# Kernel optimization log

Hardware: AMD Instinct MI355X
Metric: run time of the kernel (lower is better)

The kernel has to match this reference:

```python
import jax, jax.numpy as jnp
import numpy as np

EMBED_DIM = 1024
N_HEADS = 16
N_KV_HEADS = 4
HEAD_DIM = EMBED_DIM // N_HEADS  # 64
N_GROUPS = N_HEADS // N_KV_HEADS  # 4
COPE_MAX_LEN = 64


def setup_inputs() -> dict:
    key = jax.random.key(0)
    ks = jax.random.split(key, 16)
    B, T = 4, 1024
    s = 0.02
    return {
        "query": jax.random.normal(ks[0], (B, T, EMBED_DIM), jnp.float32),
        "key": jax.random.normal(ks[1], (B, T, EMBED_DIM), jnp.float32),
        "value": jax.random.normal(ks[2], (B, T, EMBED_DIM), jnp.float32),
        "wq": jax.random.normal(ks[3], (EMBED_DIM, EMBED_DIM), jnp.float32) * s,
        "bq": jnp.zeros((EMBED_DIM,), jnp.float32),
        "wk": jax.random.normal(ks[4], (HEAD_DIM * N_KV_HEADS, EMBED_DIM), jnp.float32) * s,
        "bk": jnp.zeros((HEAD_DIM * N_KV_HEADS,), jnp.float32),
        "wv": jax.random.normal(ks[5], (HEAD_DIM * N_KV_HEADS, EMBED_DIM), jnp.float32) * s,
        "bv": jnp.zeros((HEAD_DIM * N_KV_HEADS,), jnp.float32),
        "wo": jax.random.normal(ks[6], (EMBED_DIM, EMBED_DIM), jnp.float32) * s,
        "bo": jnp.zeros((EMBED_DIM,), jnp.float32),
        "pos_emb": jax.random.normal(ks[7], (HEAD_DIM, COPE_MAX_LEN), jnp.float32) * s,
    }


def _cope_bias(q, sim, pos_emb):
    # q: [b,g,h,i,d], sim: [b,g,h,i,j], pos_emb: [d, M]
    gates = jax.nn.sigmoid(sim)
    # reversed cumulative sum over keys -> contextual positions
    pos = jnp.flip(jnp.cumsum(jnp.flip(gates, -1), axis=-1), -1)
    pos = jnp.clip(pos, 0.0, COPE_MAX_LEN - 1)
    pos_floor = jnp.floor(pos)
    w = pos - pos_floor  # interpolation weight
    logits_int = jnp.einsum('bghid,dm->bghim', q, pos_emb)  # [b,g,h,i,M]
    lo = jnp.take_along_axis(logits_int, pos_floor.astype(jnp.int32), axis=-1)
    hi = jnp.take_along_axis(logits_int, jnp.ceil(pos).astype(jnp.int32), axis=-1)
    return hi * w + lo * (1.0 - w)


def reference(query, key, value, wq, bq, wk, bk, wv, bv, wo, bo, pos_emb):
    B, Tq, E = query.shape
    Tk = key.shape[1]
    temp = jnp.sqrt(jnp.float32(HEAD_DIM))
    q = (query @ wq.T + bq).reshape(B, Tq, N_HEADS, HEAD_DIM).transpose(0, 2, 1, 3)
    k = (key @ wk.T + bk).reshape(B, Tk, N_KV_HEADS, HEAD_DIM).transpose(0, 2, 1, 3)
    v = (value @ wv.T + bv).reshape(B, Tk, N_KV_HEADS, HEAD_DIM).transpose(0, 2, 1, 3)
    qg = q.reshape(B, N_GROUPS, N_KV_HEADS, Tq, HEAD_DIM)
    sim = jnp.einsum('bghid,bhjd->bghij', qg, k) / temp
    attn_weights = sim + _cope_bias(qg, sim, pos_emb)
    attn_probs = jax.nn.softmax(attn_weights.astype(jnp.float32), axis=-1).astype(attn_weights.dtype)
    out = jnp.einsum('bghij,bhjd->bghid', attn_probs, v)
    # b g h i d -> b i (g h) d -> b i E
    out = out.transpose(0, 3, 1, 2, 4).reshape(B, Tq, E)
    return out @ wo.T + bo
```

## Files before the change

kernel.cpp:

```cpp
#include <hip/hip_runtime.h>
#include <hip/hip_bf16.h>
#include <stdint.h>

typedef unsigned short u16;
typedef __attribute__((ext_vector_type(8))) short short8;
typedef __attribute__((ext_vector_type(4))) float f32x4;

#define BB 4
#define TT 1024
#define EE 1024
#define NH 16
#define NKV 4
#define HD 64
#define KVD 256
#define SR 1028

__device__ inline u16 f2bf(float f) {
    uint32_t u = __float_as_uint(f);
    uint32_t r = u + 0x7fffu + ((u >> 16) & 1u);
    return (u16)(r >> 16);
}

__device__ inline f32x4 mfma16(short8 a, short8 b, f32x4 c) {
    return __builtin_amdgcn_mfma_f32_16x16x32_bf16(a, b, c, 0, 0, 0);
}

__device__ inline int simsIdx(int row, int col) {
    return row * SR + (col ^ (((col >> 5) & 7) << 2));
}

__device__ inline void gload16(const u16* g, u16* l) {
    __builtin_amdgcn_global_load_lds((const __attribute__((address_space(1))) void*)g,
                                     (__attribute__((address_space(3))) void*)l, 16, 0, 0);
}

__device__ inline void cast8(const float* s, u16* d) {
    const f32x4* p = (const f32x4*)s;
    f32x4 x = p[0], y = p[1];
    short8 v = (short8){(short)f2bf(x[0]), (short)f2bf(x[1]), (short)f2bf(x[2]), (short)f2bf(x[3]),
                        (short)f2bf(y[0]), (short)f2bf(y[1]), (short)f2bf(y[2]), (short)f2bf(y[3])};
    *(short8*)d = v;
}

__global__ __launch_bounds__(256) void cast_all(
    const float* s0, u16* d0, int n0, const float* s1, u16* d1, int n1,
    const float* s2, u16* d2, int n2, const float* s3, u16* d3, int n3,
    const float* s4, u16* d4, int n4, const float* s5, u16* d5, int n5,
    const float* s6, u16* d6, int n6)
{
    int u = blockIdx.x * 256 + threadIdx.x;
    const float* s; u16* d; int off = u;
    if      (off < n0)              { s = s0; d = d0; }
    else if ((off -= n0) < n1)      { s = s1; d = d1; }
    else if ((off -= n1) < n2)      { s = s2; d = d2; }
    else if ((off -= n2) < n3)      { s = s3; d = d3; }
    else if ((off -= n3) < n4)      { s = s4; d = d4; }
    else if ((off -= n4) < n5)      { s = s5; d = d5; }
    else if ((off -= n5) < n6)      { s = s6; d = d6; }
    else return;
    cast8(s + (size_t)off * 8, d + (size_t)off * 8);
}

__global__ __launch_bounds__(256) void cast_posT(const float* __restrict__ pe, u16* __restrict__ PT) {
    int t = blockIdx.x * 256 + threadIdx.x;
    PT[t] = f2bf(pe[(t & 63) * 64 + (t >> 6)]);
}

template<int BM, int BN>
__device__ inline void gemm_core(const u16* __restrict__ A, const u16* __restrict__ W,
                                 int K, int bm, int bn, u16* As, u16* Bs,
                                 f32x4 (&acc)[BM / 32][BN / 32])
{
    const int t = threadIdx.x, l = t & 63, w = t >> 6;
    const int wr = w >> 1, wc = w & 1, lc = l & 15, lg = l >> 4;
    const int lr8 = l >> 3;
    const int c8s = (l & 7) ^ lr8;
    constexpr int FI = BM / 32, FJ = BN / 32;
    constexpr int NCA = BM / 8, NCW = BN / 8;

    for (int k0 = 0; k0 < K; k0 += 64) {
        #pragma unroll
        for (int r = 0; r < NCA / 4; ++r) {
            int chunk = w * (NCA / 4) + r;
            gload16(&A[(size_t)(bm + chunk * 8 + lr8) * K + k0 + c8s * 8], &As[chunk * 512]);
        }
        #pragma unroll
        for (int r = 0; r < NCW / 4; ++r) {
            int chunk = w * (NCW / 4) + r;
            gload16(&W[(size_t)(bn + chunk * 8 + lr8) * K + k0 + c8s * 8], &Bs[chunk * 512]);
        }
        __syncthreads();
        #pragma unroll
        for (int ks = 0; ks < 2; ++ks) {
            short8 af[FI], bfr[FJ];
            #pragma unroll
            for (int fi = 0; fi < FI; ++fi) {
                int row = wr * (BM / 2) + fi * 16 + lc;
                af[fi] = *(const short8*)((const char*)As +
                           ((row * 128 + (ks * 32 + lg * 8) * 2) ^ ((row & 7) << 4)));
            }
            #pragma unroll
            for (int fj = 0; fj < FJ; ++fj) {
                int row = wc * (BN / 2) + fj * 16 + lc;
                bfr[fj] = *(const short8*)((const char*)Bs +
                            ((row * 128 + (ks * 32 + lg * 8) * 2) ^ ((row & 7) << 4)));
            }
            #pragma unroll
            for (int fi = 0; fi < FI; ++fi)
                #pragma unroll
                for (int fj = 0; fj < FJ; ++fj)
                    acc[fi][fj] = mfma16(af[fi], bfr[fj], acc[fi][fj]);
        }
        __syncthreads();
    }
}

template<int BM, int BN>
__global__ __launch_bounds__(256) void gemm_bf16(const u16* __restrict__ A,
                                                 const u16* __restrict__ W,
                                                 const float* __restrict__ bias,
                                                 float* __restrict__ Cf, u16* __restrict__ Ch,
                                                 int M, int N, int K)
{
    __shared__ u16 As[BM * 64], Bs[BN * 64];
    const int bm = blockIdx.y * BM, bn = blockIdx.x * BN;
    const int l = threadIdx.x & 63, w = threadIdx.x >> 6;
    const int wr = w >> 1, wc = w & 1, lc = l & 15, lg = l >> 4;
    constexpr int FI = BM / 32, FJ = BN / 32;

    f32x4 acc[FI][FJ];
    #pragma unroll
    for (int i = 0; i < FI; ++i)
        #pragma unroll
        for (int j = 0; j < FJ; ++j) acc[i][j] = (f32x4){0.f, 0.f, 0.f, 0.f};

    gemm_core<BM, BN>(A, W, K, bm, bn, As, Bs, acc);

    #pragma unroll
    for (int fj = 0; fj < FJ; ++fj) {
        int col = bn + wc * (BN / 2) + fj * 16 + lc;
        float bv = bias[col];
        #pragma unroll
        for (int fi = 0; fi < FI; ++fi)
            #pragma unroll
            for (int r = 0; r < 4; ++r) {
                int row = bm + wr * (BM / 2) + fi * 16 + lg * 4 + r;
                float v = acc[fi][fj][r] + bv;
                if (Cf) Cf[(size_t)row * N + col] = v;
                else    Ch[(size_t)row * N + col] = f2bf(v);
            }
    }
}

__global__ __launch_bounds__(256) void kv_gemm(const u16* __restrict__ Ki, const u16* __restrict__ Vi,
                                               const u16* __restrict__ Wk, const u16* __restrict__ Wv,
                                               const float* __restrict__ bk, const float* __restrict__ bv,
                                               u16* __restrict__ Kh, u16* __restrict__ VhT)
{
    __shared__ u16 As[64 * 64], Bs[64 * 64];
    const int by = blockIdx.y;
    const bool isV = by >= 64;
    const u16* A = isV ? Vi : Ki;
    const u16* W = isV ? Wv : Wk;
    const float* bias = isV ? bv : bk;
    const int bm = (isV ? by - 64 : by) * 64, bn = blockIdx.x * 64;
    const int l = threadIdx.x & 63, w = threadIdx.x >> 6;
    const int wr = w >> 1, wc = w & 1, lc = l & 15, lg = l >> 4;

    f32x4 acc[2][2];
    #pragma unroll
    for (int i = 0; i < 2; ++i)
        #pragma unroll
        for (int j = 0; j < 2; ++j) acc[i][j] = (f32x4){0.f, 0.f, 0.f, 0.f};

    gemm_core<64, 64>(A, W, EE, bm, bn, As, Bs, acc);

    #pragma unroll
    for (int fj = 0; fj < 2; ++fj) {
        int col = bn + wc * 32 + fj * 16 + lc;
        float bvv = bias[col];
        #pragma unroll
        for (int fi = 0; fi < 2; ++fi)
            #pragma unroll
            for (int r = 0; r < 4; ++r) {
                int row = bm + wr * 32 + fi * 16 + lg * 4 + r;
                float v = acc[fi][fj][r] + bvv;
                if (!isV) {
                    Kh[(size_t)row * KVD + col] = f2bf(v);
                } else {
                    int bb = row >> 10, tt = row & 1023, kv = col >> 6, d = col & 63;
                    VhT[(size_t)((bb * NKV + kv) * HD + d) * TT + tt] = f2bf(v);
                }
            }
    }
}

__global__ __launch_bounds__(256) void attn_mfma(const u16* __restrict__ Qh,
                                                 const u16* __restrict__ Kh,
                                                 const u16* __restrict__ VhT,
                                                 const u16* __restrict__ PT,
                                                 u16* __restrict__ AOh)
{
    __shared__ float sims[16 * SR];
    __shared__ float li[16 * 65];
    __shared__ float rinv[16];

    const int blk = blockIdx.x;
    const int it = blk & 63, bh = blk >> 6;
    const int head = bh & 15, b = bh >> 4, kvh = head & 3;
    const int i0 = it * 16;
    const int t = threadIdx.x, l = t & 63, w = t >> 6;
    const int lc = l & 15, lg = l >> 4;

    short8 qf[2];
    #pragma unroll
    for (int kk = 0; kk < 2; ++kk)
        qf[kk] = *(const short8*)(Qh + (size_t)(b * TT + i0 + lc) * EE + head * HD + kk * 32 + lg * 8);

    {
        f32x4 a = {0.f, 0.f, 0.f, 0.f};
        #pragma unroll
        for (int kk = 0; kk < 2; ++kk) {
            short8 bfr = *(const short8*)(PT + (w * 16 + lc) * 64 + kk * 32 + lg * 8);
            a = mfma16(qf[kk], bfr, a);
        }
        #pragma unroll
        for (int r = 0; r < 4; ++r) li[(lg * 4 + r) * 65 + w * 16 + lc] = a[r];
    }
    if (t < 16) li[t * 65 + 64] = 0.f;

    const u16* kb = Kh + (size_t)(b * TT) * KVD + kvh * HD;
    #pragma unroll 2
    for (int jt = 0; jt < 16; ++jt) {
        const int j0 = jt * 64 + w * 16;
        const u16* kr = kb + (size_t)(j0 + lc) * KVD;
        short8 k0v = *(const short8*)(kr + lg * 8);
        short8 k1v = *(const short8*)(kr + 32 + lg * 8);
        f32x4 a = {0.f, 0.f, 0.f, 0.f};
        a = mfma16(qf[0], k0v, a);
        a = mfma16(qf[1], k1v, a);
        #pragma unroll
        for (int r = 0; r < 4; ++r)
            sims[simsIdx(lg * 4 + r, j0 + lc)] = a[r] * 0.125f;
    }
    __syncthreads();

    #pragma unroll 1
    for (int rr = 0; rr < 4; ++rr) {
        const int i = w * 4 + rr;
        float sv[16];
        #pragma unroll
        for (int q = 0; q < 4; ++q) {
            f32x4 x = *(const f32x4*)&sims[simsIdx(i, l * 16 + q * 4)];
            sv[q * 4 + 0] = x[0]; sv[q * 4 + 1] = x[1];
            sv[q * 4 + 2] = x[2]; sv[q * 4 + 3] = x[3];
        }
        float lexcl[16];
        float ex = 0.f;
        #pragma unroll
        for (int k = 0; k < 16; ++k) {
            lexcl[k] = ex;
            ex += __fdividef(1.f, 1.f + __expf(-sv[k]));
        }
        float v = ex;
        #pragma unroll
        for (int off = 1; off < 64; off <<= 1) {
            float n = __shfl_up(v, off, 64);
            if (l >= off) v += n;
        }
        const float total = __shfl(v, 63, 64);
        const float lexb = v - ex;
        const float* lp = &li[i * 65];
        float rmax = -1e30f;
        #pragma unroll
        for (int k = 0; k < 16; ++k) {
            float pos = total - (lexb + lexcl[k]);
            pos = fminf(fmaxf(pos, 0.f), 63.f);
            float pf = floorf(pos);
            float wt = pos - pf;
            int lo = (int)pf;
            float l0 = lp[lo], l1 = lp[lo + 1];
            sv[k] += l0 + wt * (l1 - l0);
            rmax = fmaxf(rmax, sv[k]);
        }
        #pragma unroll
        for (int off = 32; off; off >>= 1) rmax = fmaxf(rmax, __shfl_xor(rmax, off, 64));
        float rsum = 0.f;
        #pragma unroll
        for (int k = 0; k < 16; ++k) { sv[k] = __expf(sv[k] - rmax); rsum += sv[k]; }
        #pragma unroll
        for (int off = 32; off; off >>= 1) rsum += __shfl_xor(rsum, off, 64);
        if (l == 0) rinv[i] = __fdividef(1.f, rsum);
        u16* sp = (u16*)sims + (size_t)i * (SR * 2) + l * 16;
        short8 p0 = (short8){(short)f2bf(sv[0]), (short)f2bf(sv[1]), (short)f2bf(sv[2]), (short)f2bf(sv[3]),
                             (short)f2bf(sv[4]), (short)f2bf(sv[5]), (short)f2bf(sv[6]), (short)f2bf(sv[7])};
        short8 p1 = (short8){(short)f2bf(sv[8]), (short)f2bf(sv[9]), (short)f2bf(sv[10]), (short)f2bf(sv[11]),
                             (short)f2bf(sv[12]), (short)f2bf(sv[13]), (short)f2bf(sv[14]), (short)f2bf(sv[15])};
        *(short8*)sp = p0;
        *(short8*)(sp + 8) = p1;
    }
    __syncthreads();

    const u16* sp = (const u16*)sims;
    const u16* vr = VhT + ((size_t)((b * NKV + kvh) * HD) + w * 16 + lc) * TT;
    f32x4 oacc = {0.f, 0.f, 0.f, 0.f};
    #pragma unroll 2
    for (int jt = 0; jt < 16; ++jt) {
        #pragma unroll
        for (int kt = 0; kt < 2; ++kt) {
            int col = jt * 64 + kt * 32 + lg * 8;
            short8 pa = *(const short8*)(sp + (size_t)lc * (SR * 2) + col);
            short8 vf = *(const short8*)(vr + col);
            oacc = mfma16(pa, vf, oacc);
        }
    }
    #pragma unroll
    for (int r = 0; r < 4; ++r) {
        float o = oacc[r] * rinv[lg * 4 + r];
        AOh[(size_t)(b * TT + i0 + lg * 4 + r) * EE + head * HD + w * 16 + lc] = f2bf(o);
    }
}

extern "C" void kernel_launch(void* const* d_in, const int* in_sizes, int n_in,
                              void* d_out, int out_size, void* d_ws, size_t ws_size,
                              hipStream_t stream)
{
    const float* query   = (const float*)d_in[0];
    const float* key     = (const float*)d_in[1];
    const float* value   = (const float*)d_in[2];
    const float* wq      = (const float*)d_in[3];
    const float* bq      = (const float*)d_in[4];
    const float* wk      = (const float*)d_in[5];
    const float* bk      = (const float*)d_in[6];
    const float* wv      = (const float*)d_in[7];
    const float* bv      = (const float*)d_in[8];
    const float* wo      = (const float*)d_in[9];
    const float* bo      = (const float*)d_in[10];
    const float* pos_emb = (const float*)d_in[11];
    float* out = (float*)d_out;

    char* wsb = (char*)d_ws;
    u16* Qh  = (u16*)(wsb);
    u16* Kh  = (u16*)(wsb + ((size_t)8  << 20));
    u16* VhT = (u16*)(wsb + ((size_t)10 << 20));
    u16* Qi  = (u16*)(wsb + ((size_t)12 << 20));
    u16* AOh = Qi;
    u16* PT  = (u16*)(wsb + ((size_t)20 << 20));
    u16* wqh = (u16*)(wsb + ((size_t)21 << 20));
    u16* wkh = (u16*)(wsb + ((size_t)23 << 20));
    u16* wvh = (u16*)(wsb + ((size_t)23 << 20) + ((size_t)512 << 10));
    u16* woh = (u16*)(wsb + ((size_t)24 << 20));
    u16* Ki  = (u16*)d_out;
    u16* Vi  = Ki + (size_t)BB * TT * EE;

    const int M = BB * TT;
    const int nQ = M * EE / 8, nW = EE * EE / 8, nS = KVD * EE / 8;
    const int totalU = 3 * nQ + 2 * nW + 2 * nS;

    cast_all<<<(totalU + 255) / 256, 256, 0, stream>>>(
        query, Qi, nQ, key, Ki, nQ, value, Vi, nQ,
        wq, wqh, nW, wo, woh, nW, wk, wkh, nS, wv, wvh, nS);
    cast_posT<<<16, 256, 0, stream>>>(pos_emb, PT);

    gemm_bf16<128, 128><<<dim3(EE / 128, M / 128), 256, 0, stream>>>(
        Qi, wqh, bq, nullptr, Qh, M, EE, EE);
    kv_gemm<<<dim3(KVD / 64, 2 * M / 64), 256, 0, stream>>>(
        Ki, Vi, wkh, wvh, bk, bv, Kh, VhT);

    attn_mfma<<<BB * NH * (TT / 16), 256, 0, stream>>>(Qh, Kh, VhT, PT, AOh);

    gemm_bf16<128, 128><<<dim3(EE / 128, M / 128), 256, 0, stream>>>(
        AOh, woh, bo, out, nullptr, M, EE, EE);
}
```

Baseline: 343.9 us.

## Rewrite CoPE attention as per-wave streaming online softmax with saturation fast path

Replaces the block-level attention kernel, which held a full 16x1024 score row set in LDS, with a per-wave kernel. Each wave walks keys from right to left, carrying the reversed gate cumulative sum and keeping an online-softmax running max, sum and output accumulator. Once every lane's carried position reaches the clamp at 63, it skips the sigmoid, prefix-scan and interpolation work and uses the constant bias li[63], which is exact under the clip. It also remaps block indices, shrinks LDS use per block for higher occupancy, prefetches the next K tile, and switches the Q and output projection GEMMs to 128x64 tiles. The trade-off is that online softmax adds rescaling work and is a more complex control flow.

Result: faster. 289.9 us (-15.7%).

```diff
diff --git a/kernel.cpp b/kernel.cpp
--- a/kernel.cpp
+++ b/kernel.cpp
@@ -3,6 +3,8 @@
 #include <stdint.h>
 
 typedef unsigned short u16;
+typedef unsigned int u32;
+typedef __attribute__((ext_vector_type(4))) short s16x4;
 typedef __attribute__((ext_vector_type(8))) short short8;
 typedef __attribute__((ext_vector_type(4))) float f32x4;
 
@@ -13,20 +15,16 @@
 #define NKV 4
 #define HD 64
 #define KVD 256
-#define SR 1028
+#define WSTRIDE 1296
 
 __device__ inline u16 f2bf(float f) {
-    uint32_t u = __float_as_uint(f);
-    uint32_t r = u + 0x7fffu + ((u >> 16) & 1u);
+    u32 u = __float_as_uint(f);
+    u32 r = u + 0x7fffu + ((u >> 16) & 1u);
     return (u16)(r >> 16);
 }
 
 __device__ inline f32x4 mfma16(short8 a, short8 b, f32x4 c) {
     return __builtin_amdgcn_mfma_f32_16x16x32_bf16(a, b, c, 0, 0, 0);
-}
-
-__device__ inline int simsIdx(int row, int col) {
-    return row * SR + (col ^ (((col >> 5) & 7) << 2));
 }
 
 __device__ inline void gload16(const u16* g, u16* l) {
@@ -195,21 +193,23 @@
     }
 }
 
-__global__ __launch_bounds__(256) void attn_mfma(const u16* __restrict__ Qh,
-                                                 const u16* __restrict__ Kh,
-                                                 const u16* __restrict__ VhT,
-                                                 const u16* __restrict__ PT,
-                                                 u16* __restrict__ AOh)
-{
-    __shared__ float sims[16 * SR];
-    __shared__ float li[16 * 65];
-    __shared__ float rinv[16];
-
-    const int blk = blockIdx.x;
-    const int it = blk & 63, bh = blk >> 6;
+__global__ __launch_bounds__(256) void attn_flash(const u16* __restrict__ Qh,
+                                                  const u16* __restrict__ Kh,
+                                                  const u16* __restrict__ VhT,
+                                                  const u16* __restrict__ PT,
+                                                  u16* __restrict__ AOh)
+{
+    __shared__ float lds_all[4 * WSTRIDE];
+    const int t = threadIdx.x, l = t & 63, w = t >> 6;
+    float* li = lds_all + w * WSTRIDE;
+    u16* pbuf = (u16*)(li + 1040);
+
+    const int bid = blockIdx.x;
+    const int wgs = (bid & 7) * 128 + (bid >> 3);
+    const int gw = wgs * 4 + w;
+    const int it = gw & 63, bh = gw >> 6;
     const int head = bh & 15, b = bh >> 4, kvh = head & 3;
     const int i0 = it * 16;
-    const int t = threadIdx.x, l = t & 63, w = t >> 6;
     const int lc = l & 15, lg = l >> 4;
 
     short8 qf[2];
@@ -217,107 +217,147 @@
     for (int kk = 0; kk < 2; ++kk)
         qf[kk] = *(const short8*)(Qh + (size_t)(b * TT + i0 + lc) * EE + head * HD + kk * 32 + lg * 8);
 
+    #pragma unroll
+    for (int ms = 0; ms < 4; ++ms) {
+        f32x4 a = {0.f, 0.f, 0.f, 0.f};
+        #pragma unroll
+        for (int kk = 0; kk < 2; ++kk)
+            a = mfma16(*(const short8*)(PT + (ms * 16 + lc) * 64 + kk * 32 + lg * 8), qf[kk], a);
+        #pragma unroll
+        for (int r = 0; r < 4; ++r)
+            li[lc * 65 + ms * 16 + lg * 4 + r] = a[r];
+    }
+    li[lc * 65 + 64] = 0.f;
+    asm volatile("" ::: "memory");
+    const float li63 = li[lc * 65 + 63];
+
+    const u16* kb = Kh + (size_t)(b * TT) * KVD + kvh * HD;
+    const u16* vb = VhT + (size_t)((b * NKV + kvh) * HD) * TT;
+
+    float mrun = -1e30f, rsum = 0.f, carry = 0.f;
+    f32x4 oacc[4];
+    #pragma unroll
+    for (int d4 = 0; d4 < 4; ++d4) oacc[d4] = (f32x4){0.f, 0.f, 0.f, 0.f};
+
+    short8 kf0, kf1, kf2, kf3;
     {
-        f32x4 a = {0.f, 0.f, 0.f, 0.f};
-        #pragma unroll
-        for (int kk = 0; kk < 2; ++kk) {
-            short8 bfr = *(const short8*)(PT + (w * 16 + lc) * 64 + kk * 32 + lg * 8);
-            a = mfma16(qf[kk], bfr, a);
-        }
-        #pragma unroll
-        for (int r = 0; r < 4; ++r) li[(lg * 4 + r) * 65 + w * 16 + lc] = a[r];
-    }
-    if (t < 16) li[t * 65 + 64] = 0.f;
-
-    const u16* kb = Kh + (size_t)(b * TT) * KVD + kvh * HD;
-    #pragma unroll 2
-    for (int jt = 0; jt < 16; ++jt) {
-        const int j0 = jt * 64 + w * 16;
-        const u16* kr = kb + (size_t)(j0 + lc) * KVD;
-        short8 k0v = *(const short8*)(kr + lg * 8);
-        short8 k1v = *(const short8*)(kr + 32 + lg * 8);
-        f32x4 a = {0.f, 0.f, 0.f, 0.f};
-        a = mfma16(qf[0], k0v, a);
-        a = mfma16(qf[1], k1v, a);
-        #pragma unroll
-        for (int r = 0; r < 4; ++r)
-            sims[simsIdx(lg * 4 + r, j0 + lc)] = a[r] * 0.125f;
-    }
-    __syncthreads();
-
-    #pragma unroll 1
-    for (int rr = 0; rr < 4; ++rr) {
-        const int i = w * 4 + rr;
-        float sv[16];
-        #pragma unroll
-        for (int q = 0; q < 4; ++q) {
-            f32x4 x = *(const f32x4*)&sims[simsIdx(i, l * 16 + q * 4)];
-            sv[q * 4 + 0] = x[0]; sv[q * 4 + 1] = x[1];
-            sv[q * 4 + 2] = x[2]; sv[q * 4 + 3] = x[3];
-        }
-        float lexcl[16];
-        float ex = 0.f;
-        #pragma unroll
-        for (int k = 0; k < 16; ++k) {
-            lexcl[k] = ex;
-            ex += __fdividef(1.f, 1.f + __expf(-sv[k]));
-        }
-        float v = ex;
-        #pragma unroll
-        for (int off = 1; off < 64; off <<= 1) {
-            float n = __shfl_up(v, off, 64);
-            if (l >= off) v += n;
-        }
-        const float total = __shfl(v, 63, 64);
-        const float lexb = v - ex;
-        const float* lp = &li[i * 65];
-        float rmax = -1e30f;
-        #pragma unroll
-        for (int k = 0; k < 16; ++k) {
-            float pos = total - (lexb + lexcl[k]);
-            pos = fminf(fmaxf(pos, 0.f), 63.f);
-            float pf = floorf(pos);
-            float wt = pos - pf;
-            int lo = (int)pf;
-            float l0 = lp[lo], l1 = lp[lo + 1];
-            sv[k] += l0 + wt * (l1 - l0);
-            rmax = fmaxf(rmax, sv[k]);
-        }
-        #pragma unroll
-        for (int off = 32; off; off >>= 1) rmax = fmaxf(rmax, __shfl_xor(rmax, off, 64));
-        float rsum = 0.f;
-        #pragma unroll
-        for (int k = 0; k < 16; ++k) { sv[k] = __expf(sv[k] - rmax); rsum += sv[k]; }
-        #pragma unroll
-        for (int off = 32; off; off >>= 1) rsum += __shfl_xor(rsum, off, 64);
-        if (l == 0) rinv[i] = __fdividef(1.f, rsum);
-        u16* sp = (u16*)sims + (size_t)i * (SR * 2) + l * 16;
-        short8 p0 = (short8){(short)f2bf(sv[0]), (short)f2bf(sv[1]), (short)f2bf(sv[2]), (short)f2bf(sv[3]),
-                             (short)f2bf(sv[4]), (short)f2bf(sv[5]), (short)f2bf(sv[6]), (short)f2bf(sv[7])};
-        short8 p1 = (short8){(short)f2bf(sv[8]), (short)f2bf(sv[9]), (short)f2bf(sv[10]), (short)f2bf(sv[11]),
-                             (short)f2bf(sv[12]), (short)f2bf(sv[13]), (short)f2bf(sv[14]), (short)f2bf(sv[15])};
-        *(short8*)sp = p0;
-        *(short8*)(sp + 8) = p1;
-    }
-    __syncthreads();
-
-    const u16* sp = (const u16*)sims;
-    const u16* vr = VhT + ((size_t)((b * NKV + kvh) * HD) + w * 16 + lc) * TT;
-    f32x4 oacc = {0.f, 0.f, 0.f, 0.f};
-    #pragma unroll 2
-    for (int jt = 0; jt < 16; ++jt) {
-        #pragma unroll
-        for (int kt = 0; kt < 2; ++kt) {
-            int col = jt * 64 + kt * 32 + lg * 8;
-            short8 pa = *(const short8*)(sp + (size_t)lc * (SR * 2) + col);
-            short8 vf = *(const short8*)(vr + col);
-            oacc = mfma16(pa, vf, oacc);
-        }
-    }
-    #pragma unroll
-    for (int r = 0; r < 4; ++r) {
-        float o = oacc[r] * rinv[lg * 4 + r];
-        AOh[(size_t)(b * TT + i0 + lg * 4 + r) * EE + head * HD + w * 16 + lc] = f2bf(o);
+        const u16* krL = kb + (size_t)(31 * 32 + lc) * KVD;
+        const u16* krH = kb + (size_t)(31 * 32 + 16 + lc) * KVD;
+        kf0 = *(const short8*)(krL + lg * 8);
+        kf1 = *(const short8*)(krL + 32 + lg * 8);
+        kf2 = *(const short8*)(krH + lg * 8);
+        kf3 = *(const short8*)(krH + 32 + lg * 8);
+    }
+
+    for (int p = 31; p >= 0; --p) {
+        const int t0 = p * 32;
+        short8 kn0 = kf0, kn1 = kf1, kn2 = kf2, kn3 = kf3;
+        if (p > 0) {
+            const u16* krL = kb + (size_t)(t0 - 32 + lc) * KVD;
+            const u16* krH = kb + (size_t)(t0 - 32 + 16 + lc) * KVD;
+            kn0 = *(const short8*)(krL + lg * 8);
+            kn1 = *(const short8*)(krL + 32 + lg * 8);
+            kn2 = *(const short8*)(krH + lg * 8);
+            kn3 = *(const short8*)(krH + 32 + lg * 8);
+        }
+        f32x4 sL4 = {0.f, 0.f, 0.f, 0.f}, sH4 = {0.f, 0.f, 0.f, 0.f};
+        sL4 = mfma16(kf0, qf[0], sL4); sL4 = mfma16(kf1, qf[1], sL4);
+        sH4 = mfma16(kf2, qf[0], sH4); sH4 = mfma16(kf3, qf[1], sH4);
+
+        float aL[4], aH[4];
+        const bool fast = __all(carry >= 63.0f);
+        if (fast) {
+            #pragma unroll
+            for (int r = 0; r < 4; ++r) {
+                aL[r] = sL4[r] * 0.125f + li63;
+                aH[r] = sH4[r] * 0.125f + li63;
+            }
+        } else {
+            float sL[4], sH[4], gL[4], gH[4];
+            #pragma unroll
+            for (int r = 0; r < 4; ++r) {
+                sL[r] = sL4[r] * 0.125f; sH[r] = sH4[r] * 0.125f;
+                gL[r] = __fdividef(1.f, 1.f + __expf(-sL[r]));
+                gH[r] = __fdividef(1.f, 1.f + __expf(-sH[r]));
+            }
+            float oh3 = gH[3], oh2 = gH[2] + oh3, oh1 = gH[1] + oh2, oh0 = gH[0] + oh1;
+            float tH = oh0;
+            float aX = __shfl_xor(tH, 16), bX = __shfl_xor(tH, 32), cX = __shfl_xor(aX, 32);
+            float hiH = (lg == 0) ? aX + bX + cX : (lg == 1) ? bX + cX : (lg == 2) ? aX : 0.f;
+            float totH = tH + aX + bX + cX;
+            float baseH = carry + hiH;
+            float carryM = carry + totH;
+            float ol3 = gL[3], ol2 = gL[2] + ol3, ol1 = gL[1] + ol2, ol0 = gL[0] + ol1;
+            float tL = ol0;
+            float aY = __shfl_xor(tL, 16), bY = __shfl_xor(tL, 32), cY = __shfl_xor(aY, 32);
+            float hiL = (lg == 0) ? aY + bY + cY : (lg == 1) ? bY + cY : (lg == 2) ? aY : 0.f;
+            float totL = tL + aY + bY + cY;
+            float baseL = carryM + hiL;
+            carry = carryM + totL;
+            const float* lp = &li[lc * 65];
+            float osf[4] = {oh0, oh1, oh2, oh3};
+            float osl[4] = {ol0, ol1, ol2, ol3};
+            #pragma unroll
+            for (int r = 0; r < 4; ++r) {
+                float pos = fminf(baseH + osf[r], 63.f);
+                float pf = floorf(pos), wt = pos - pf;
+                int lo = (int)pf;
+                float l0 = lp[lo], l1 = lp[lo + 1];
+                aH[r] = sH[r] + l0 + wt * (l1 - l0);
+            }
+            #pragma unroll
+            for (int r = 0; r < 4; ++r) {
+                float pos = fminf(baseL + osl[r], 63.f);
+                float pf = floorf(pos), wt = pos - pf;
+                int lo = (int)pf;
+                float l0 = lp[lo], l1 = lp[lo + 1];
+                aL[r] = sL[r] + l0 + wt * (l1 - l0);
+            }
+        }
+        float mt = fmaxf(fmaxf(fmaxf(aL[0], aL[1]), fmaxf(aL[2], aL[3])),
+                         fmaxf(fmaxf(aH[0], aH[1]), fmaxf(aH[2], aH[3])));
+        mt = fmaxf(mt, __shfl_xor(mt, 16));
+        mt = fmaxf(mt, __shfl_xor(mt, 32));
+        float mnew = fmaxf(mrun, mt);
+        float sc = __expf(mrun - mnew);
+        float pL[4], pH[4];
+        float ts = 0.f;
+        #pragma unroll
+        for (int r = 0; r < 4; ++r) {
+            pL[r] = __expf(aL[r] - mnew); ts += pL[r];
+            pH[r] = __expf(aH[r] - mnew); ts += pH[r];
+        }
+        ts += __shfl_xor(ts, 16);
+        ts += __shfl_xor(ts, 32);
+        rsum = rsum * sc + ts;
+        if (__any(mt > mrun)) {
+            #pragma unroll
+            for (int d4 = 0; d4 < 4; ++d4) {
+                oacc[d4][0] *= sc; oacc[d4][1] *= sc; oacc[d4][2] *= sc; oacc[d4][3] *= sc;
+            }
+        }
+        mrun = mnew;
+        s16x4 w0 = (s16x4){(short)f2bf(pL[0]), (short)f2bf(pL[1]), (short)f2bf(pL[2]), (short)f2bf(pL[3])};
+        s16x4 w1 = (s16x4){(short)f2bf(pH[0]), (short)f2bf(pH[1]), (short)f2bf(pH[2]), (short)f2bf(pH[3])};
+        *(s16x4*)((char*)pbuf + lc * 64 + lg * 8)      = w0;
+        *(s16x4*)((char*)pbuf + lc * 64 + 32 + lg * 8) = w1;
+        asm volatile("" ::: "memory");
+        short8 pfrag = *(const short8*)((const char*)pbuf + lc * 64 + lg * 16);
+        asm volatile("" ::: "memory");
+        #pragma unroll
+        for (int d4 = 0; d4 < 4; ++d4)
+            oacc[d4] = mfma16(*(const short8*)(vb + (size_t)(d4 * 16 + lc) * TT + t0 + lg * 8),
+                              pfrag, oacc[d4]);
+        kf0 = kn0; kf1 = kn1; kf2 = kn2; kf3 = kn3;
+    }
+
+    const float rinv = __fdividef(1.f, rsum);
+    u16* ob = AOh + (size_t)(b * TT + i0 + lc) * EE + head * HD + lg * 4;
+    #pragma unroll
+    for (int d4 = 0; d4 < 4; ++d4) {
+        s16x4 pk = (s16x4){(short)f2bf(oacc[d4][0] * rinv), (short)f2bf(oacc[d4][1] * rinv),
+                           (short)f2bf(oacc[d4][2] * rinv), (short)f2bf(oacc[d4][3] * rinv)};
+        *(s16x4*)(ob + d4 * 16) = pk;
     }
 }
 
@@ -362,13 +402,13 @@
         wq, wqh, nW, wo, woh, nW, wk, wkh, nS, wv, wvh, nS);
     cast_posT<<<16, 256, 0, stream>>>(pos_emb, PT);
 
-    gemm_bf16<128, 128><<<dim3(EE / 128, M / 128), 256, 0, stream>>>(
+    gemm_bf16<128, 64><<<dim3(EE / 64, M / 128), 256, 0, stream>>>(
         Qi, wqh, bq, nullptr, Qh, M, EE, EE);
     kv_gemm<<<dim3(KVD / 64, 2 * M / 64), 256, 0, stream>>>(
         Ki, Vi, wkh, wvh, bk, bv, Kh, VhT);
 
-    attn_mfma<<<BB * NH * (TT / 16), 256, 0, stream>>>(Qh, Kh, VhT, PT, AOh);
-
-    gemm_bf16<128, 128><<<dim3(EE / 128, M / 128), 256, 0, stream>>>(
+    attn_flash<<<BB * NH * (TT / 16) / 4, 256, 0, stream>>>(Qh, Kh, VhT, PT, AOh);
+
+    gemm_bf16<128, 64><<<dim3(EE / 64, M / 128), 256, 0, stream>>>(
         AOh, woh, bo, out, nullptr, M, EE, EE);
 }
```
